# Kernel tuning notes

Measured on AMD Instinct MI355X. Metric: run time of the kernel, lower is better.

Reference implementation:

```python
import jax, jax.numpy as jnp
import numpy as np

N = 100000      # nodes
E = 1600000     # edges
NFEAT = 128
NHID = 32
NHEADS = 8
NCLASS = 40
K = 2           # hop_num
BETA = 0.1      # diffusion teleport weight
ALPHA = 0.2     # leaky relu slope


def setup_inputs() -> dict:
    key = jax.random.key(0)
    ks = jax.random.split(key, 8)
    x = jax.random.normal(ks[0], (N, NFEAT), dtype=jnp.float32)
    edge_index = jax.random.randint(ks[1], (2, E), 0, N, dtype=jnp.int64)
    W = jax.random.normal(ks[2], (NHEADS, NFEAT, NHID), dtype=jnp.float32) * 0.1
    a_src = jax.random.normal(ks[3], (NHEADS, NHID), dtype=jnp.float32) * 0.1
    a_dst = jax.random.normal(ks[4], (NHEADS, NHID), dtype=jnp.float32) * 0.1
    W_out = jax.random.normal(ks[5], (NHEADS * NHID, NCLASS), dtype=jnp.float32) * 0.1
    a_src_out = jax.random.normal(ks[6], (NCLASS,), dtype=jnp.float32) * 0.1
    a_dst_out = jax.random.normal(ks[7], (NCLASS,), dtype=jnp.float32) * 0.1
    return {"x": x, "edge_index": edge_index, "W": W, "a_src": a_src,
            "a_dst": a_dst, "W_out": W_out, "a_src_out": a_src_out,
            "a_dst_out": a_dst_out}


def _khop_attention(h0, src, dst, a_s, a_d):
    """One sparse k-hop attention head. h0: [N, D] transformed features."""
    s = h0 @ a_s            # [N]
    t = h0 @ a_d            # [N]
    e = jax.nn.leaky_relu(s[src] + t[dst], ALPHA)          # [E]
    # numerically stable per-destination softmax over incoming edges
    m = jax.ops.segment_max(e, dst, num_segments=N)        # [N]
    m = jnp.where(jnp.isfinite(m), m, 0.0)                 # empty segments -> -inf
    p = jnp.exp(e - m[dst])                                # [E]
    denom = jax.ops.segment_sum(p, dst, num_segments=N) + 1e-16
    w = p / denom[dst]                                     # [E] attention coeffs
    # k-hop decaying diffusion: feat <- (1-beta)*A_att feat + beta*h0
    feat = h0
    for _ in range(K):
        msg = jax.ops.segment_sum(w[:, None] * feat[src], dst, num_segments=N)
        feat = (1.0 - BETA) * msg + BETA * h0
    return feat


def reference(x, edge_index, W, a_src, a_dst, W_out, a_src_out, a_dst_out):
    src, dst = edge_index[0], edge_index[1]
    # multi-head layer (concat=True -> elu per head, concat along features)
    heads = [jax.nn.elu(_khop_attention(x @ W[i], src, dst, a_src[i], a_dst[i]))
             for i in range(NHEADS)]
    h = jnp.concatenate(heads, axis=1)                     # [N, NHEADS*NHID]
    # output attention layer (concat=False -> raw output)
    out = _khop_attention(h @ W_out, src, dst, a_src_out, a_dst_out)  # [N, NCLASS]
    return jax.nn.log_softmax(jax.nn.elu(out), axis=1)
```

## Files before the change

### kernel.cpp

```cpp
#include <hip/hip_runtime.h>
#include <hip/hip_fp16.h>
#include <stdint.h>

#define NN      100000
#define EE      1600000
#define NFEATC  128
#define NHIDC   32
#define NHEADSC 8
#define NCLASSC 40
#define FDIM    256
#define NBLK    ((NN+255)/256)

typedef unsigned short u16;
typedef __attribute__((ext_vector_type(8))) short bf16x8;
typedef __attribute__((ext_vector_type(4))) float f32x4;

__device__ __forceinline__ float b2f(u16 u){ union{uint32_t i; float f;} v; v.i=((uint32_t)u)<<16; return v.f; }
__device__ __forceinline__ float lof(uint32_t u){ union{uint32_t i; float f;} v; v.i=u<<16; return v.f; }
__device__ __forceinline__ float hif(uint32_t u){ union{uint32_t i; float f;} v; v.i=u&0xFFFF0000u; return v.f; }
__device__ __forceinline__ u16 f2b(float f){ union{float f; uint32_t i;} v; v.f=f; uint32_t x=v.i; return (u16)((x + 0x7FFFu + ((x>>16)&1u))>>16); }
__device__ __forceinline__ uint32_t pack2(float a, float b){ return (uint32_t)f2b(a) | ((uint32_t)f2b(b)<<16); }
__device__ __forceinline__ float lrelu(float e){ return e > 0.f ? e : 0.2f*e; }

__global__ __launch_bounds__(256) void k_transposeW(const float* __restrict__ W, u16* __restrict__ Wt){
  int i = blockIdx.x*256 + threadIdx.x;
  if (i >= FDIM*NFEATC) return;
  int c = i >> 7, k = i & 127;
  int head = c >> 5, hid = c & 31;
  Wt[c*NFEATC + k] = f2b(W[head*(NFEATC*NHIDC) + k*NHIDC + hid]);
}

__global__ __launch_bounds__(256) void k_gemm1_mfma(const float* __restrict__ x, const u16* __restrict__ Wt,
                                                    u16* __restrict__ h0){
  int w = threadIdx.x >> 6, lane = threadIdx.x & 63;
  int nt = blockIdx.x;
  int m = lane & 15, q = lane >> 4;
  int row = nt*16 + m;
  int c0 = w*64;
  const float* xrow = x + (size_t)row*NFEATC;
  f32x4 acc0 = {0.f,0.f,0.f,0.f}, acc1 = {0.f,0.f,0.f,0.f};
  f32x4 acc2 = {0.f,0.f,0.f,0.f}, acc3 = {0.f,0.f,0.f,0.f};
  #pragma unroll
  for (int kk=0; kk<NFEATC; kk+=32){
    int ko = kk + q*8;
    float4 xa = *(const float4*)(xrow + ko);
    float4 xb = *(const float4*)(xrow + ko + 4);
    bf16x8 a;
    a[0]=(short)f2b(xa.x); a[1]=(short)f2b(xa.y); a[2]=(short)f2b(xa.z); a[3]=(short)f2b(xa.w);
    a[4]=(short)f2b(xb.x); a[5]=(short)f2b(xb.y); a[6]=(short)f2b(xb.z); a[7]=(short)f2b(xb.w);
    bf16x8 b0 = *(const bf16x8*)(Wt + (size_t)(c0 +  0 + m)*NFEATC + ko);
    bf16x8 b1 = *(const bf16x8*)(Wt + (size_t)(c0 + 16 + m)*NFEATC + ko);
    bf16x8 b2 = *(const bf16x8*)(Wt + (size_t)(c0 + 32 + m)*NFEATC + ko);
    bf16x8 b3 = *(const bf16x8*)(Wt + (size_t)(c0 + 48 + m)*NFEATC + ko);
    acc0 = __builtin_amdgcn_mfma_f32_16x16x32_bf16(a, b0, acc0, 0,0,0);
    acc1 = __builtin_amdgcn_mfma_f32_16x16x32_bf16(a, b1, acc1, 0,0,0);
    acc2 = __builtin_amdgcn_mfma_f32_16x16x32_bf16(a, b2, acc2, 0,0,0);
    acc3 = __builtin_amdgcn_mfma_f32_16x16x32_bf16(a, b3, acc3, 0,0,0);
  }
  #pragma unroll
  for (int r=0; r<4; r++){
    size_t base = (size_t)(nt*16 + q*4 + r)*FDIM + c0 + m;
    h0[base +  0] = f2b(acc0[r]);
    h0[base + 16] = f2b(acc1[r]);
    h0[base + 32] = f2b(acc2[r]);
    h0[base + 48] = f2b(acc3[r]);
  }
}

__global__ __launch_bounds__(256) void k_st(const u16* __restrict__ h0, const float* __restrict__ a_src,
                                            const float* __restrict__ a_dst, u16* __restrict__ s,
                                            u16* __restrict__ t_){
  int i = blockIdx.x*256 + threadIdx.x;
  if (i >= NN*NHEADSC) return;
  int n = i>>3, head = i&7;
  const u16* hp = h0 + (size_t)n*FDIM + head*NHIDC;
  const float* ap = a_src + head*NHIDC;
  const float* bp = a_dst + head*NHIDC;
  float ss=0.f, tt=0.f;
  #pragma unroll
  for (int j=0;j<NHIDC;j++){
    float h = b2f(hp[j]);
    ss = fmaf(h, ap[j], ss); tt = fmaf(h, bp[j], tt);
  }
  s[i]=f2b(ss); t_[i]=f2b(tt);
}

__global__ __launch_bounds__(256) void k_zero(int* __restrict__ p, int n){
  int i = blockIdx.x*256 + threadIdx.x;
  if (i < n) p[i] = 0;
}
__global__ __launch_bounds__(256) void k_zero_f(float* __restrict__ p, int n){
  int i = blockIdx.x*256 + threadIdx.x;
  if (i < n) p[i] = 0.f;
}
__global__ __launch_bounds__(256) void k_count(const int* __restrict__ dst, int* __restrict__ counts){
  int e = blockIdx.x*256 + threadIdx.x;
  if (e < EE) atomicAdd(&counts[dst[e]], 1);
}
__global__ __launch_bounds__(256) void k_blocksum(const int* __restrict__ counts, int* __restrict__ bsum){
  __shared__ int wsum[4];
  int b = blockIdx.x, t = threadIdx.x;
  int i = b*256 + t;
  int v = (i < NN) ? counts[i] : 0;
  #pragma unroll
  for (int off=32; off; off>>=1) v += __shfl_xor(v, off);
  if ((t & 63) == 0) wsum[t>>6] = v;
  __syncthreads();
  if (t == 0) bsum[b] = wsum[0]+wsum[1]+wsum[2]+wsum[3];
}
__global__ __launch_bounds__(512) void k_scan_bsum(const int* __restrict__ bsum, int* __restrict__ boff){
  __shared__ int lds[512];
  int t = threadIdx.x;
  int v = (t < NBLK) ? bsum[t] : 0;
  lds[t] = v; __syncthreads();
  for (int off=1; off<512; off<<=1){
    int u = (t>=off) ? lds[t-off] : 0;
    __syncthreads();
    lds[t] += u;
    __syncthreads();
  }
  if (t < NBLK) boff[t] = lds[t] - v;
}
__global__ __launch_bounds__(256) void k_scan_final(const int* __restrict__ counts, const int* __restrict__ boff,
                                                    int* __restrict__ row_start){
  __shared__ int lds[256];
  int b = blockIdx.x, t = threadIdx.x;
  int i = b*256 + t;
  int v = (i < NN) ? counts[i] : 0;
  lds[t] = v; __syncthreads();
  for (int off=1; off<256; off<<=1){
    int u = (t>=off) ? lds[t-off] : 0;
    __syncthreads();
    lds[t] += u;
    __syncthreads();
  }
  if (i < NN) row_start[i] = boff[b] + lds[t] - v;
  if (b == 0 && t == 0) row_start[NN] = EE;
}
__global__ __launch_bounds__(256) void k_scatter(const int* __restrict__ src, const int* __restrict__ dst,
                                                 const int* __restrict__ row_start, int* __restrict__ fill,
                                                 int* __restrict__ csr_src){
  int e = blockIdx.x*256 + threadIdx.x;
  if (e >= EE) return;
  int d = dst[e];
  int pos = row_start[d] + atomicAdd(&fill[d], 1);
  csr_src[pos] = src[e];
}

__global__ __launch_bounds__(256) void k_att(const u16* __restrict__ s, const u16* __restrict__ t_,
                                             const int* __restrict__ row_start, const int* __restrict__ csr_src,
                                             u16* __restrict__ p_all, __half* __restrict__ scale){
  int i = blockIdx.x*256 + threadIdx.x;
  if (i >= NN*NHEADSC) return;
  int n = i>>3, head = i&7;
  int beg = row_start[n], end = row_start[n+1];
  float tn = b2f(t_[i]);
  float d0=0.f,d1=0.f,d2=0.f,d3=0.f;
  int pos = beg;
  for (; pos+4<=end; pos+=4){
    int u0=csr_src[pos], u1=csr_src[pos+1], u2=csr_src[pos+2], u3=csr_src[pos+3];
    float e0=lrelu(b2f(s[u0*NHEADSC+head])+tn);
    float e1=lrelu(b2f(s[u1*NHEADSC+head])+tn);
    float e2=lrelu(b2f(s[u2*NHEADSC+head])+tn);
    float e3=lrelu(b2f(s[u3*NHEADSC+head])+tn);
    u16 p0=f2b(__expf(e0)), p1=f2b(__expf(e1)), p2=f2b(__expf(e2)), p3=f2b(__expf(e3));
    p_all[(size_t)(pos+0)*NHEADSC+head]=p0;
    p_all[(size_t)(pos+1)*NHEADSC+head]=p1;
    p_all[(size_t)(pos+2)*NHEADSC+head]=p2;
    p_all[(size_t)(pos+3)*NHEADSC+head]=p3;
    d0+=b2f(p0); d1+=b2f(p1); d2+=b2f(p2); d3+=b2f(p3);
  }
  for (; pos<end; pos++){
    int u = csr_src[pos];
    float e = lrelu(b2f(s[u*NHEADSC+head])+tn);
    u16 pb = f2b(__expf(e));
    p_all[(size_t)pos*NHEADSC+head]=pb;
    d0 += b2f(pb);
  }
  scale[i] = __float2half(1.0f/(((d0+d1)+(d2+d3)) + 1e-16f));
}

#define ACC8(p, g) \
  a0=fmaf(p,lof(g.x),a0); a1=fmaf(p,hif(g.x),a1); \
  a2=fmaf(p,lof(g.y),a2); a3=fmaf(p,hif(g.y),a3); \
  a4=fmaf(p,lof(g.z),a4); a5=fmaf(p,hif(g.z),a5); \
  a6=fmaf(p,lof(g.w),a6); a7=fmaf(p,hif(g.w),a7);

__global__ __launch_bounds__(256) void k_hop1(const u16* __restrict__ h0, const u16* __restrict__ p_all,
                                              const __half* __restrict__ scale, const int* __restrict__ row_start,
                                              const int* __restrict__ csr_src, u16* __restrict__ featA){
  int wv = threadIdx.x >> 6, l = threadIdx.x & 63;
  int n = blockIdx.x*4 + wv;
  int half = l >> 5, sl = l & 31;
  int cg = 8*sl;
  int head = sl >> 2;
  float sc_ = __half2float(scale[n*NHEADSC + head]);
  int beg = row_start[n], end = row_start[n+1];
  float a0=0.f,a1=0.f,a2=0.f,a3=0.f,a4=0.f,a5=0.f,a6=0.f,a7=0.f;
  int pos = beg;
  for (; pos+8<=end; pos+=8){
    int e0=csr_src[pos+0+half], e1=csr_src[pos+2+half], e2=csr_src[pos+4+half], e3=csr_src[pos+6+half];
    float p0=b2f(p_all[(size_t)(pos+0+half)*NHEADSC+head]);
    float p1=b2f(p_all[(size_t)(pos+2+half)*NHEADSC+head]);
    float p2=b2f(p_all[(size_t)(pos+4+half)*NHEADSC+head]);
    float p3=b2f(p_all[(size_t)(pos+6+half)*NHEADSC+head]);
    uint4 g0 = *(const uint4*)(h0 + (size_t)e0*FDIM + cg);
    uint4 g1 = *(const uint4*)(h0 + (size_t)e1*FDIM + cg);
    uint4 g2 = *(const uint4*)(h0 + (size_t)e2*FDIM + cg);
    uint4 g3 = *(const uint4*)(h0 + (size_t)e3*FDIM + cg);
    ACC8(p0, g0) ACC8(p1, g1) ACC8(p2, g2) ACC8(p3, g3)
  }
  for (; pos+2<=end; pos+=2){
    int e = csr_src[pos+half];
    float p = b2f(p_all[(size_t)(pos+half)*NHEADSC+head]);
    uint4 g = *(const uint4*)(h0 + (size_t)e*FDIM + cg);
    ACC8(p, g)
  }
  if (pos < end && half == 0){
    int e = csr_src[pos];
    float p = b2f(p_all[(size_t)pos*NHEADSC+head]);
    uint4 g = *(const uint4*)(h0 + (size_t)e*FDIM + cg);
    ACC8(p, g)
  }
  a0 += __shfl_xor(a0, 32); a1 += __shfl_xor(a1, 32);
  a2 += __shfl_xor(a2, 32); a3 += __shfl_xor(a3, 32);
  a4 += __shfl_xor(a4, 32); a5 += __shfl_xor(a5, 32);
  a6 += __shfl_xor(a6, 32); a7 += __shfl_xor(a7, 32);
  if (half == 0){
    uint4 hu = *(const uint4*)(h0 + (size_t)n*FDIM + cg);
    float r0 = 0.9f*sc_*a0 + 0.1f*lof(hu.x);
    float r1 = 0.9f*sc_*a1 + 0.1f*hif(hu.x);
    float r2 = 0.9f*sc_*a2 + 0.1f*lof(hu.y);
    float r3 = 0.9f*sc_*a3 + 0.1f*hif(hu.y);
    float r4 = 0.9f*sc_*a4 + 0.1f*lof(hu.z);
    float r5 = 0.9f*sc_*a5 + 0.1f*hif(hu.z);
    float r6 = 0.9f*sc_*a6 + 0.1f*lof(hu.w);
    float r7 = 0.9f*sc_*a7 + 0.1f*hif(hu.w);
    uint4 o;
    o.x = pack2(r0,r1); o.y = pack2(r2,r3); o.z = pack2(r4,r5); o.w = pack2(r6,r7);
    *(uint4*)(featA + (size_t)n*FDIM + cg) = o;
  }
}

__global__ __launch_bounds__(256) void k_hop2(const u16* __restrict__ featA, const u16* __restrict__ h0,
                                              const u16* __restrict__ p_all, const __half* __restrict__ scale,
                                              const int* __restrict__ row_start, const int* __restrict__ csr_src,
                                              const float* __restrict__ W_out, float* __restrict__ out0){
  __shared__ float hs[4][FDIM+4];
  int wv = threadIdx.x >> 6, l = threadIdx.x & 63;
  int n = blockIdx.x*4 + wv;
  int half = l >> 5, sl = l & 31;
  int cg = 8*sl;
  int head = sl >> 2;
  float sc_ = __half2float(scale[n*NHEADSC + head]);
  int beg = row_start[n], end = row_start[n+1];
  float a0=0.f,a1=0.f,a2=0.f,a3=0.f,a4=0.f,a5=0.f,a6=0.f,a7=0.f;
  int pos = beg;
  for (; pos+8<=end; pos+=8){
    int e0=csr_src[pos+0+half], e1=csr_src[pos+2+half], e2=csr_src[pos+4+half], e3=csr_src[pos+6+half];
    float p0=b2f(p_all[(size_t)(pos+0+half)*NHEADSC+head]);
    float p1=b2f(p_all[(size_t)(pos+2+half)*NHEADSC+head]);
    float p2=b2f(p_all[(size_t)(pos+4+half)*NHEADSC+head]);
    float p3=b2f(p_all[(size_t)(pos+6+half)*NHEADSC+head]);
    uint4 g0 = *(const uint4*)(featA + (size_t)e0*FDIM + cg);
    uint4 g1 = *(const uint4*)(featA + (size_t)e1*FDIM + cg);
    uint4 g2 = *(const uint4*)(featA + (size_t)e2*FDIM + cg);
    uint4 g3 = *(const uint4*)(featA + (size_t)e3*FDIM + cg);
    ACC8(p0, g0) ACC8(p1, g1) ACC8(p2, g2) ACC8(p3, g3)
  }
  for (; pos+2<=end; pos+=2){
    int e = csr_src[pos+half];
    float p = b2f(p_all[(size_t)(pos+half)*NHEADSC+head]);
    uint4 g = *(const uint4*)(featA + (size_t)e*FDIM + cg);
    ACC8(p, g)
  }
  if (pos < end && half == 0){
    int e = csr_src[pos];
    float p = b2f(p_all[(size_t)pos*NHEADSC+head]);
    uint4 g = *(const uint4*)(featA + (size_t)e*FDIM + cg);
    ACC8(p, g)
  }
  a0 += __shfl_xor(a0, 32); a1 += __shfl_xor(a1, 32);
  a2 += __shfl_xor(a2, 32); a3 += __shfl_xor(a3, 32);
  a4 += __shfl_xor(a4, 32); a5 += __shfl_xor(a5, 32);
  a6 += __shfl_xor(a6, 32); a7 += __shfl_xor(a7, 32);
  if (half == 0){
    uint4 hu = *(const uint4*)(h0 + (size_t)n*FDIM + cg);
    float r0 = 0.9f*sc_*a0 + 0.1f*lof(hu.x);
    float r1 = 0.9f*sc_*a1 + 0.1f*hif(hu.x);
    float r2 = 0.9f*sc_*a2 + 0.1f*lof(hu.y);
    float r3 = 0.9f*sc_*a3 + 0.1f*hif(hu.y);
    float r4 = 0.9f*sc_*a4 + 0.1f*lof(hu.z);
    float r5 = 0.9f*sc_*a5 + 0.1f*hif(hu.z);
    float r6 = 0.9f*sc_*a6 + 0.1f*lof(hu.w);
    float r7 = 0.9f*sc_*a7 + 0.1f*hif(hu.w);
    hs[wv][cg  ] = r0 > 0.f ? r0 : (__expf(r0)-1.0f);
    hs[wv][cg+1] = r1 > 0.f ? r1 : (__expf(r1)-1.0f);
    hs[wv][cg+2] = r2 > 0.f ? r2 : (__expf(r2)-1.0f);
    hs[wv][cg+3] = r3 > 0.f ? r3 : (__expf(r3)-1.0f);
    hs[wv][cg+4] = r4 > 0.f ? r4 : (__expf(r4)-1.0f);
    hs[wv][cg+5] = r5 > 0.f ? r5 : (__expf(r5)-1.0f);
    hs[wv][cg+6] = r6 > 0.f ? r6 : (__expf(r6)-1.0f);
    hs[wv][cg+7] = r7 > 0.f ? r7 : (__expf(r7)-1.0f);
  }
  __syncthreads();
  int t = threadIdx.x;
  if (t < 4*NCLASSC){
    int node = t/NCLASSC, c = t%NCLASSC;
    const float* hv = hs[node];
    const float* wp = W_out + c;
    float o = 0.f;
    #pragma unroll 8
    for (int k=0;k<FDIM;k++) o = fmaf(hv[k], wp[(size_t)k*NCLASSC], o);
    out0[(size_t)(blockIdx.x*4+node)*NCLASSC + c] = o;
  }
}

__global__ __launch_bounds__(256) void k_st_out(const float* __restrict__ out0, const float* __restrict__ a_s,
                                                const float* __restrict__ a_d, float* __restrict__ s,
                                                float* __restrict__ t_){
  int n = blockIdx.x*256 + threadIdx.x;
  if (n >= NN) return;
  const float* r = out0 + (size_t)n*NCLASSC;
  float ss=0.f, tt=0.f;
  for (int c=0;c<NCLASSC;c++){ float v=r[c]; ss=fmaf(v,a_s[c],ss); tt=fmaf(v,a_d[c],tt); }
  s[n]=ss; t_[n]=tt;
}

__global__ __launch_bounds__(256) void k_att_out(const float* __restrict__ s, const float* __restrict__ t_,
                                                 const int* __restrict__ row_start, const int* __restrict__ csr_src,
                                                 float* __restrict__ p_out, float* __restrict__ scale_out){
  int n = blockIdx.x*256 + threadIdx.x;
  if (n >= NN) return;
  int beg = row_start[n], end = row_start[n+1];
  float tn = t_[n];
  float d0=0.f,d1=0.f,d2=0.f,d3=0.f;
  int pos = beg;
  for (; pos+4<=end; pos+=4){
    int u0=csr_src[pos], u1=csr_src[pos+1], u2=csr_src[pos+2], u3=csr_src[pos+3];
    float p0=__expf(lrelu(s[u0]+tn));
    float p1=__expf(lrelu(s[u1]+tn));
    float p2=__expf(lrelu(s[u2]+tn));
    float p3=__expf(lrelu(s[u3]+tn));
    p_out[pos]=p0; p_out[pos+1]=p1; p_out[pos+2]=p2; p_out[pos+3]=p3;
    d0+=p0; d1+=p1; d2+=p2; d3+=p3;
  }
  for (; pos<end; pos++){
    float p = __expf(lrelu(s[csr_src[pos]]+tn));
    p_out[pos] = p;
    d0 += p;
  }
  scale_out[n] = 1.0f/(((d0+d1)+(d2+d3)) + 1e-16f);
}

__global__ __launch_bounds__(64) void k_hop1_out(const float* __restrict__ out0, const float* __restrict__ p_out,
                                                 const float* __restrict__ scale_out, const int* __restrict__ row_start,
                                                 const int* __restrict__ csr_src, u16* __restrict__ outA){
  int n = blockIdx.x, t = threadIdx.x;
  float sc_ = scale_out[n];
  int beg = row_start[n], end = row_start[n+1];
  int tc = (t < NCLASSC) ? t : 0;
  float a0=0.f,a1=0.f,a2=0.f,a3=0.f;
  int pos = beg;
  for (; pos+4<=end; pos+=4){
    int u0=csr_src[pos], u1=csr_src[pos+1], u2=csr_src[pos+2], u3=csr_src[pos+3];
    float p0=p_out[pos], p1=p_out[pos+1], p2=p_out[pos+2], p3=p_out[pos+3];
    float f0=out0[(size_t)u0*NCLASSC+tc];
    float f1=out0[(size_t)u1*NCLASSC+tc];
    float f2=out0[(size_t)u2*NCLASSC+tc];
    float f3=out0[(size_t)u3*NCLASSC+tc];
    a0=fmaf(p0,f0,a0); a1=fmaf(p1,f1,a1); a2=fmaf(p2,f2,a2); a3=fmaf(p3,f3,a3);
  }
  for (; pos<end; pos++){
    a0=fmaf(p_out[pos], out0[(size_t)csr_src[pos]*NCLASSC+tc], a0);
  }
  if (t < NCLASSC){
    float res = 0.9f*sc_*((a0+a1)+(a2+a3)) + 0.1f*out0[(size_t)n*NCLASSC + t];
    outA[(size_t)n*NCLASSC + t] = f2b(res);
  }
}

__global__ __launch_bounds__(64) void k_hop2_out_final(const u16* __restrict__ outA, const float* __restrict__ out0,
                                                       const float* __restrict__ p_out, const float* __restrict__ scale_out,
                                                       const int* __restrict__ row_start, const int* __restrict__ csr_src,
                                                       float* __restrict__ out){
  int n = blockIdx.x, t = threadIdx.x;
  float sc_ = scale_out[n];
  int beg = row_start[n], end = row_start[n+1];
  int tc = (t < NCLASSC) ? t : 0;
  float a0=0.f,a1=0.f,a2=0.f,a3=0.f;
  int pos = beg;
  for (; pos+4<=end; pos+=4){
    int u0=csr_src[pos], u1=csr_src[pos+1], u2=csr_src[pos+2], u3=csr_src[pos+3];
    float p0=p_out[pos], p1=p_out[pos+1], p2=p_out[pos+2], p3=p_out[pos+3];
    float f0=b2f(outA[(size_t)u0*NCLASSC+tc]);
    float f1=b2f(outA[(size_t)u1*NCLASSC+tc]);
    float f2=b2f(outA[(size_t)u2*NCLASSC+tc]);
    float f3=b2f(outA[(size_t)u3*NCLASSC+tc]);
    a0=fmaf(p0,f0,a0); a1=fmaf(p1,f1,a1); a2=fmaf(p2,f2,a2); a3=fmaf(p3,f3,a3);
  }
  for (; pos<end; pos++){
    a0=fmaf(p_out[pos], b2f(outA[(size_t)csr_src[pos]*NCLASSC+tc]), a0);
  }
  float v = -1e30f;
  if (t < NCLASSC){
    float res = 0.9f*sc_*((a0+a1)+(a2+a3)) + 0.1f*out0[(size_t)n*NCLASSC + t];
    v = res > 0.f ? res : (__expf(res)-1.0f);
  }
  float m = v;
  #pragma unroll
  for (int off=32; off; off>>=1) m = fmaxf(m, __shfl_xor(m, off));
  float ex = (t < NCLASSC) ? __expf(v - m) : 0.f;
  float ssum = ex;
  #pragma unroll
  for (int off=32; off; off>>=1) ssum += __shfl_xor(ssum, off);
  if (t < NCLASSC) out[(size_t)n*NCLASSC + t] = v - m - __logf(ssum);
}

extern "C" void kernel_launch(void* const* d_in, const int* in_sizes, int n_in,
                              void* d_out, int out_size, void* d_ws, size_t ws_size,
                              hipStream_t stream){
  const float* x        = (const float*)d_in[0];
  const int*   ei       = (const int*)d_in[1];
  const float* W        = (const float*)d_in[2];
  const float* a_src    = (const float*)d_in[3];
  const float* a_dst    = (const float*)d_in[4];
  const float* W_out    = (const float*)d_in[5];
  const float* a_src_o  = (const float*)d_in[6];
  const float* a_dst_o  = (const float*)d_in[7];
  float* out            = (float*)d_out;
  const int* e_src = ei;
  const int* e_dst = ei + EE;

  char* ws = (char*)d_ws;
  size_t off = 0;
  auto alloc = [&](size_t bytes)->char*{ char* p = ws + off; off += (bytes + 255) & ~(size_t)255; return p; };

  u16*    h0        = (u16*)   alloc((size_t)NN*FDIM*2);
  u16*    featA     = (u16*)   alloc((size_t)NN*FDIM*2);
  float*  out0      = (float*) alloc((size_t)NN*NCLASSC*4);
  int*    csr_src   = (int*)   alloc((size_t)EE*4);
  int*    row_start = (int*)   alloc((size_t)(NN+1)*4);
  char*   regS      =          alloc((size_t)NN*NHEADSC*2*2);
  u16*    p_all     = (u16*)   alloc((size_t)EE*NHEADSC*2);
  __half* scale     = (__half*)alloc((size_t)NN*NHEADSC*2);
  int*    counts    = (int*)   alloc((size_t)NN*4);
  int*    bsum      = (int*)   alloc((size_t)NBLK*4);
  int*    boff      = (int*)   alloc((size_t)NBLK*4);
  u16*    Wt        = (u16*)   alloc((size_t)FDIM*NFEATC*2);

  u16*   s         = (u16*)regS;
  u16*   t_        = (u16*)(regS + (size_t)NN*NHEADSC*2);
  float* s_out     = (float*)regS;
  float* t_out     = s_out + NN;
  float* scale_out = t_out + NN;
  u16*   outA      = (u16*)featA;
  float* p_out     = (float*)p_all;

  k_transposeW<<<(FDIM*NFEATC+255)/256, 256, 0, stream>>>(W, Wt);
  k_gemm1_mfma<<<NN/16, 256, 0, stream>>>(x, Wt, h0);
  k_st<<<(NN*NHEADSC+255)/256, 256, 0, stream>>>(h0, a_src, a_dst, s, t_);

  k_zero<<<(NN+255)/256, 256, 0, stream>>>(counts, NN);
  k_count<<<(EE+255)/256, 256, 0, stream>>>(e_dst, counts);
  k_blocksum<<<NBLK, 256, 0, stream>>>(counts, bsum);
  k_scan_bsum<<<1, 512, 0, stream>>>(bsum, boff);
  k_scan_final<<<NBLK, 256, 0, stream>>>(counts, boff, row_start);
  k_zero<<<(NN+255)/256, 256, 0, stream>>>(counts, NN);
  k_scatter<<<(EE+255)/256, 256, 0, stream>>>(e_src, e_dst, row_start, counts, csr_src);

  k_att<<<(NN*NHEADSC+255)/256, 256, 0, stream>>>(s, t_, row_start, csr_src, p_all, scale);
  k_hop1<<<NN/4, 256, 0, stream>>>(h0, p_all, scale, row_start, csr_src, featA);
  k_hop2<<<NN/4, 256, 0, stream>>>(featA, h0, p_all, scale, row_start, csr_src, W_out, out0);

  k_st_out<<<(NN+255)/256, 256, 0, stream>>>(out0, a_src_o, a_dst_o, s_out, t_out);
  k_att_out<<<(NN+255)/256, 256, 0, stream>>>(s_out, t_out, row_start, csr_src, p_out, scale_out);
  k_hop1_out<<<NN, 64, 0, stream>>>(out0, p_out, scale_out, row_start, csr_src, outA);
  k_hop2_out_final<<<NN, 64, 0, stream>>>(outA, out0, p_out, scale_out, row_start, csr_src, out);
}
```

Before: 845.5 us.

## Split hop kernels into two feature-half passes with prefetched neighbor indices

Each hop kernel now runs twice, and each pass covers half of the 256-wide feature vector. The gathered working set per pass (25.6 MB of bf16 rows) is meant to fit better in L2/MALL. The gather loop uses four edge groups of 16 lanes, prefetches the next csr_src indices a step ahead, and masks the tail instead of using remainder loops. The output projection reads a transposed W_out with float4 loads and accumulates the two passes into out0 with a read-modify-write. In exchange, csr_src, p_all and scale are read twice and two extra kernel launches are added.

```diff
diff --git a/kernel.cpp b/kernel.cpp
--- a/kernel.cpp
+++ b/kernel.cpp
@@ -28,6 +28,13 @@
   int c = i >> 7, k = i & 127;
   int head = c >> 5, hid = c & 31;
   Wt[c*NFEATC + k] = f2b(W[head*(NFEATC*NHIDC) + k*NHIDC + hid]);
+}
+
+__global__ __launch_bounds__(256) void k_transposeWout(const float* __restrict__ W_out, float* __restrict__ Wo_t){
+  int i = blockIdx.x*256 + threadIdx.x;
+  if (i >= FDIM*NCLASSC) return;
+  int c = i / FDIM, k = i % FDIM;
+  Wo_t[i] = W_out[(size_t)k*NCLASSC + c];
 }
 
 __global__ __launch_bounds__(256) void k_gemm1_mfma(const float* __restrict__ x, const u16* __restrict__ Wt,
@@ -89,10 +96,6 @@
   int i = blockIdx.x*256 + threadIdx.x;
   if (i < n) p[i] = 0;
 }
-__global__ __launch_bounds__(256) void k_zero_f(float* __restrict__ p, int n){
-  int i = blockIdx.x*256 + threadIdx.x;
-  if (i < n) p[i] = 0.f;
-}
 __global__ __launch_bounds__(256) void k_count(const int* __restrict__ dst, int* __restrict__ counts){
   int e = blockIdx.x*256 + threadIdx.x;
   if (e < EE) atomicAdd(&counts[dst[e]], 1);
@@ -186,47 +189,41 @@
   a4=fmaf(p,lof(g.z),a4); a5=fmaf(p,hif(g.z),a5); \
   a6=fmaf(p,lof(g.w),a6); a7=fmaf(p,hif(g.w),a7);
 
-__global__ __launch_bounds__(256) void k_hop1(const u16* __restrict__ h0, const u16* __restrict__ p_all,
-                                              const __half* __restrict__ scale, const int* __restrict__ row_start,
-                                              const int* __restrict__ csr_src, u16* __restrict__ featA){
+__global__ __launch_bounds__(256) void k_hop1_split(const u16* __restrict__ h0, const u16* __restrict__ p_all,
+                                                    const __half* __restrict__ scale, const int* __restrict__ row_start,
+                                                    const int* __restrict__ csr_src, u16* __restrict__ featA,
+                                                    int pass){
   int wv = threadIdx.x >> 6, l = threadIdx.x & 63;
   int n = blockIdx.x*4 + wv;
-  int half = l >> 5, sl = l & 31;
-  int cg = 8*sl;
-  int head = sl >> 2;
+  int g = l >> 4, il = l & 15;
+  int cg = pass*128 + il*8;
+  int head = cg >> 5;
   float sc_ = __half2float(scale[n*NHEADSC + head]);
   int beg = row_start[n], end = row_start[n+1];
   float a0=0.f,a1=0.f,a2=0.f,a3=0.f,a4=0.f,a5=0.f,a6=0.f,a7=0.f;
-  int pos = beg;
-  for (; pos+8<=end; pos+=8){
-    int e0=csr_src[pos+0+half], e1=csr_src[pos+2+half], e2=csr_src[pos+4+half], e3=csr_src[pos+6+half];
-    float p0=b2f(p_all[(size_t)(pos+0+half)*NHEADSC+head]);
-    float p1=b2f(p_all[(size_t)(pos+2+half)*NHEADSC+head]);
-    float p2=b2f(p_all[(size_t)(pos+4+half)*NHEADSC+head]);
-    float p3=b2f(p_all[(size_t)(pos+6+half)*NHEADSC+head]);
+  int e0,e1;
+  {
+    int v0=beg+g, v1=beg+4+g;
+    int c0=csr_src[v0<EE?v0:EE-1], c1=csr_src[v1<EE?v1:EE-1];
+    e0 = v0<end?c0:n; e1 = v1<end?c1:n;
+  }
+  for (int pos=beg; pos<end; pos+=8){
+    int w0=pos+8+g, w1=pos+12+g;
+    int c0=csr_src[w0<EE?w0:EE-1], c1=csr_src[w1<EE?w1:EE-1];
+    int q0 = (pos+g  )<EE ? (pos+g  ) : EE-1;
+    int q1 = (pos+4+g)<EE ? (pos+4+g) : EE-1;
+    float pv0 = (pos+g   < end) ? b2f(p_all[(size_t)q0*NHEADSC+head]) : 0.f;
+    float pv1 = (pos+4+g < end) ? b2f(p_all[(size_t)q1*NHEADSC+head]) : 0.f;
     uint4 g0 = *(const uint4*)(h0 + (size_t)e0*FDIM + cg);
     uint4 g1 = *(const uint4*)(h0 + (size_t)e1*FDIM + cg);
-    uint4 g2 = *(const uint4*)(h0 + (size_t)e2*FDIM + cg);
-    uint4 g3 = *(const uint4*)(h0 + (size_t)e3*FDIM + cg);
-    ACC8(p0, g0) ACC8(p1, g1) ACC8(p2, g2) ACC8(p3, g3)
-  }
-  for (; pos+2<=end; pos+=2){
-    int e = csr_src[pos+half];
-    float p = b2f(p_all[(size_t)(pos+half)*NHEADSC+head]);
-    uint4 g = *(const uint4*)(h0 + (size_t)e*FDIM + cg);
-    ACC8(p, g)
-  }
-  if (pos < end && half == 0){
-    int e = csr_src[pos];
-    float p = b2f(p_all[(size_t)pos*NHEADSC+head]);
-    uint4 g = *(const uint4*)(h0 + (size_t)e*FDIM + cg);
-    ACC8(p, g)
-  }
-  a0 += __shfl_xor(a0, 32); a1 += __shfl_xor(a1, 32);
-  a2 += __shfl_xor(a2, 32); a3 += __shfl_xor(a3, 32);
-  a4 += __shfl_xor(a4, 32); a5 += __shfl_xor(a5, 32);
-  a6 += __shfl_xor(a6, 32); a7 += __shfl_xor(a7, 32);
-  if (half == 0){
+    ACC8(pv0,g0) ACC8(pv1,g1)
+    e0 = w0<end?c0:n; e1 = w1<end?c1:n;
+  }
+  a0 += __shfl_xor(a0,16); a1 += __shfl_xor(a1,16); a2 += __shfl_xor(a2,16); a3 += __shfl_xor(a3,16);
+  a4 += __shfl_xor(a4,16); a5 += __shfl_xor(a5,16); a6 += __shfl_xor(a6,16); a7 += __shfl_xor(a7,16);
+  a0 += __shfl_xor(a0,32); a1 += __shfl_xor(a1,32); a2 += __shfl_xor(a2,32); a3 += __shfl_xor(a3,32);
+  a4 += __shfl_xor(a4,32); a5 += __shfl_xor(a5,32); a6 += __shfl_xor(a6,32); a7 += __shfl_xor(a7,32);
+  if (l < 16){
     uint4 hu = *(const uint4*)(h0 + (size_t)n*FDIM + cg);
     float r0 = 0.9f*sc_*a0 + 0.1f*lof(hu.x);
     float r1 = 0.9f*sc_*a1 + 0.1f*hif(hu.x);
@@ -242,49 +239,43 @@
   }
 }
 
-__global__ __launch_bounds__(256) void k_hop2(const u16* __restrict__ featA, const u16* __restrict__ h0,
-                                              const u16* __restrict__ p_all, const __half* __restrict__ scale,
-                                              const int* __restrict__ row_start, const int* __restrict__ csr_src,
-                                              const float* __restrict__ W_out, float* __restrict__ out0){
-  __shared__ float hs[4][FDIM+4];
+__global__ __launch_bounds__(256) void k_hop2_split(const u16* __restrict__ featA, const u16* __restrict__ h0,
+                                                    const u16* __restrict__ p_all, const __half* __restrict__ scale,
+                                                    const int* __restrict__ row_start, const int* __restrict__ csr_src,
+                                                    const float* __restrict__ Wo_t, float* __restrict__ out0,
+                                                    int pass){
+  __shared__ __align__(16) float hs[4][132];
   int wv = threadIdx.x >> 6, l = threadIdx.x & 63;
   int n = blockIdx.x*4 + wv;
-  int half = l >> 5, sl = l & 31;
-  int cg = 8*sl;
-  int head = sl >> 2;
+  int g = l >> 4, il = l & 15;
+  int cg = pass*128 + il*8;
+  int head = cg >> 5;
   float sc_ = __half2float(scale[n*NHEADSC + head]);
   int beg = row_start[n], end = row_start[n+1];
   float a0=0.f,a1=0.f,a2=0.f,a3=0.f,a4=0.f,a5=0.f,a6=0.f,a7=0.f;
-  int pos = beg;
-  for (; pos+8<=end; pos+=8){
-    int e0=csr_src[pos+0+half], e1=csr_src[pos+2+half], e2=csr_src[pos+4+half], e3=csr_src[pos+6+half];
-    float p0=b2f(p_all[(size_t)(pos+0+half)*NHEADSC+head]);
-    float p1=b2f(p_all[(size_t)(pos+2+half)*NHEADSC+head]);
-    float p2=b2f(p_all[(size_t)(pos+4+half)*NHEADSC+head]);
-    float p3=b2f(p_all[(size_t)(pos+6+half)*NHEADSC+head]);
+  int e0,e1;
+  {
+    int v0=beg+g, v1=beg+4+g;
+    int c0=csr_src[v0<EE?v0:EE-1], c1=csr_src[v1<EE?v1:EE-1];
+    e0 = v0<end?c0:n; e1 = v1<end?c1:n;
+  }
+  for (int pos=beg; pos<end; pos+=8){
+    int w0=pos+8+g, w1=pos+12+g;
+    int c0=csr_src[w0<EE?w0:EE-1], c1=csr_src[w1<EE?w1:EE-1];
+    int q0 = (pos+g  )<EE ? (pos+g  ) : EE-1;
+    int q1 = (pos+4+g)<EE ? (pos+4+g) : EE-1;
+    float pv0 = (pos+g   < end) ? b2f(p_all[(size_t)q0*NHEADSC+head]) : 0.f;
+    float pv1 = (pos+4+g < end) ? b2f(p_all[(size_t)q1*NHEADSC+head]) : 0.f;
     uint4 g0 = *(const uint4*)(featA + (size_t)e0*FDIM + cg);
     uint4 g1 = *(const uint4*)(featA + (size_t)e1*FDIM + cg);
-    uint4 g2 = *(const uint4*)(featA + (size_t)e2*FDIM + cg);
-    uint4 g3 = *(const uint4*)(featA + (size_t)e3*FDIM + cg);
-    ACC8(p0, g0) ACC8(p1, g1) ACC8(p2, g2) ACC8(p3, g3)
-  }
-  for (; pos+2<=end; pos+=2){
-    int e = csr_src[pos+half];
-    float p = b2f(p_all[(size_t)(pos+half)*NHEADSC+head]);
-    uint4 g = *(const uint4*)(featA + (size_t)e*FDIM + cg);
-    ACC8(p, g)
-  }
-  if (pos < end && half == 0){
-    int e = csr_src[pos];
-    float p = b2f(p_all[(size_t)pos*NHEADSC+head]);
-    uint4 g = *(const uint4*)(featA + (size_t)e*FDIM + cg);
-    ACC8(p, g)
-  }
-  a0 += __shfl_xor(a0, 32); a1 += __shfl_xor(a1, 32);
-  a2 += __shfl_xor(a2, 32); a3 += __shfl_xor(a3, 32);
-  a4 += __shfl_xor(a4, 32); a5 += __shfl_xor(a5, 32);
-  a6 += __shfl_xor(a6, 32); a7 += __shfl_xor(a7, 32);
-  if (half == 0){
+    ACC8(pv0,g0) ACC8(pv1,g1)
+    e0 = w0<end?c0:n; e1 = w1<end?c1:n;
+  }
+  a0 += __shfl_xor(a0,16); a1 += __shfl_xor(a1,16); a2 += __shfl_xor(a2,16); a3 += __shfl_xor(a3,16);
+  a4 += __shfl_xor(a4,16); a5 += __shfl_xor(a5,16); a6 += __shfl_xor(a6,16); a7 += __shfl_xor(a7,16);
+  a0 += __shfl_xor(a0,32); a1 += __shfl_xor(a1,32); a2 += __shfl_xor(a2,32); a3 += __shfl_xor(a3,32);
+  a4 += __shfl_xor(a4,32); a5 += __shfl_xor(a5,32); a6 += __shfl_xor(a6,32); a7 += __shfl_xor(a7,32);
+  if (l < 16){
     uint4 hu = *(const uint4*)(h0 + (size_t)n*FDIM + cg);
     float r0 = 0.9f*sc_*a0 + 0.1f*lof(hu.x);
     float r1 = 0.9f*sc_*a1 + 0.1f*hif(hu.x);
@@ -294,25 +285,36 @@
     float r5 = 0.9f*sc_*a5 + 0.1f*hif(hu.z);
     float r6 = 0.9f*sc_*a6 + 0.1f*lof(hu.w);
     float r7 = 0.9f*sc_*a7 + 0.1f*hif(hu.w);
-    hs[wv][cg  ] = r0 > 0.f ? r0 : (__expf(r0)-1.0f);
-    hs[wv][cg+1] = r1 > 0.f ? r1 : (__expf(r1)-1.0f);
-    hs[wv][cg+2] = r2 > 0.f ? r2 : (__expf(r2)-1.0f);
-    hs[wv][cg+3] = r3 > 0.f ? r3 : (__expf(r3)-1.0f);
-    hs[wv][cg+4] = r4 > 0.f ? r4 : (__expf(r4)-1.0f);
-    hs[wv][cg+5] = r5 > 0.f ? r5 : (__expf(r5)-1.0f);
-    hs[wv][cg+6] = r6 > 0.f ? r6 : (__expf(r6)-1.0f);
-    hs[wv][cg+7] = r7 > 0.f ? r7 : (__expf(r7)-1.0f);
+    float4 ha, hb;
+    ha.x = r0 > 0.f ? r0 : (__expf(r0)-1.0f);
+    ha.y = r1 > 0.f ? r1 : (__expf(r1)-1.0f);
+    ha.z = r2 > 0.f ? r2 : (__expf(r2)-1.0f);
+    ha.w = r3 > 0.f ? r3 : (__expf(r3)-1.0f);
+    hb.x = r4 > 0.f ? r4 : (__expf(r4)-1.0f);
+    hb.y = r5 > 0.f ? r5 : (__expf(r5)-1.0f);
+    hb.z = r6 > 0.f ? r6 : (__expf(r6)-1.0f);
+    hb.w = r7 > 0.f ? r7 : (__expf(r7)-1.0f);
+    *(float4*)&hs[wv][il*8  ] = ha;
+    *(float4*)&hs[wv][il*8+4] = hb;
   }
   __syncthreads();
   int t = threadIdx.x;
   if (t < 4*NCLASSC){
     int node = t/NCLASSC, c = t%NCLASSC;
     const float* hv = hs[node];
-    const float* wp = W_out + c;
-    float o = 0.f;
+    const float* wt = Wo_t + (size_t)c*FDIM + pass*128;
+    float o0=0.f,o1=0.f,o2=0.f,o3=0.f;
     #pragma unroll 8
-    for (int k=0;k<FDIM;k++) o = fmaf(hv[k], wp[(size_t)k*NCLASSC], o);
-    out0[(size_t)(blockIdx.x*4+node)*NCLASSC + c] = o;
+    for (int k=0;k<128;k+=4){
+      float4 h4 = *(const float4*)(hv + k);
+      float4 w4 = *(const float4*)(wt + k);
+      o0=fmaf(h4.x,w4.x,o0); o1=fmaf(h4.y,w4.y,o1);
+      o2=fmaf(h4.z,w4.z,o2); o3=fmaf(h4.w,w4.w,o3);
+    }
+    float o = (o0+o1)+(o2+o3);
+    size_t oi = (size_t)(blockIdx.x*4+node)*NCLASSC + c;
+    if (pass == 0) out0[oi] = o;
+    else           out0[oi] += o;
   }
 }
 
@@ -448,6 +450,7 @@
   int*    bsum      = (int*)   alloc((size_t)NBLK*4);
   int*    boff      = (int*)   alloc((size_t)NBLK*4);
   u16*    Wt        = (u16*)   alloc((size_t)FDIM*NFEATC*2);
+  float*  Wo_t      = (float*) alloc((size_t)FDIM*NCLASSC*4);
 
   u16*   s         = (u16*)regS;
   u16*   t_        = (u16*)(regS + (size_t)NN*NHEADSC*2);
@@ -458,6 +461,7 @@
   float* p_out     = (float*)p_all;
 
   k_transposeW<<<(FDIM*NFEATC+255)/256, 256, 0, stream>>>(W, Wt);
+  k_transposeWout<<<(FDIM*NCLASSC+255)/256, 256, 0, stream>>>(W_out, Wo_t);
   k_gemm1_mfma<<<NN/16, 256, 0, stream>>>(x, Wt, h0);
   k_st<<<(NN*NHEADSC+255)/256, 256, 0, stream>>>(h0, a_src, a_dst, s, t_);
 
@@ -470,8 +474,10 @@
   k_scatter<<<(EE+255)/256, 256, 0, stream>>>(e_src, e_dst, row_start, counts, csr_src);
 
   k_att<<<(NN*NHEADSC+255)/256, 256, 0, stream>>>(s, t_, row_start, csr_src, p_all, scale);
-  k_hop1<<<NN/4, 256, 0, stream>>>(h0, p_all, scale, row_start, csr_src, featA);
-  k_hop2<<<NN/4, 256, 0, stream>>>(featA, h0, p_all, scale, row_start, csr_src, W_out, out0);
+  k_hop1_split<<<NN/4, 256, 0, stream>>>(h0, p_all, scale, row_start, csr_src, featA, 0);
+  k_hop1_split<<<NN/4, 256, 0, stream>>>(h0, p_all, scale, row_start, csr_src, featA, 1);
+  k_hop2_split<<<NN/4, 256, 0, stream>>>(featA, h0, p_all, scale, row_start, csr_src, Wo_t, out0, 0);
+  k_hop2_split<<<NN/4, 256, 0, stream>>>(featA, h0, p_all, scale, row_start, csr_src, Wo_t, out0, 1);
 
   k_st_out<<<(NN+255)/256, 256, 0, stream>>>(out0, a_src_o, a_dst_o, s_out, t_out);
   k_att_out<<<(NN+255)/256, 256, 0, stream>>>(s_out, t_out, row_start, csr_src, p_out, scale_out);
```

After: 1.184 ms. +40.1%, slower.
